# Optimization experiments

Measured on AMD Instinct MI355X. Metric: run time of the kernel, lower is better.

Reference implementation:

```python
import jax, jax.numpy as jnp
import numpy as np

B, N, E, T = 32768, 6, 6, 2  # batch graphs, nodes, edges (ring), edge types
H, DIN = 128, 3


def _ring_rel():
    # off_diag[i, (i+1)%N] = 1 -> edge e: sender i, receiver (i+1)%N
    send = np.arange(N)
    recv = (np.arange(N) + 1) % N
    eye = np.eye(N, dtype=np.float32)
    return jnp.asarray(eye[recv]), jnp.asarray(eye[send])  # rel_rec, rel_send [E,N]


def setup_inputs() -> dict:
    key = jax.random.key(0)
    ks = iter(jax.random.split(key, 40))
    rn = lambda shape, s=0.1: jax.random.normal(next(ks), shape, jnp.float32) * s
    rel_rec, rel_send = _ring_rel()
    inp = {
        'x': rn((B, N, DIN), 1.0),
        'rel_rec': rel_rec, 'rel_send': rel_send,
        'e1w1': rn((DIN, H)), 'e1b1': jnp.full((H,), 0.1), 'e1w2': rn((H, H)), 'e1b2': jnp.full((H,), 0.1),
        'e2w1': rn((2 * H, H)), 'e2b1': jnp.full((H,), 0.1), 'e2w2': rn((H, H)), 'e2b2': jnp.full((H,), 0.1),
        'e3w1': rn((H, H)), 'e3b1': jnp.full((H,), 0.1), 'e3w2': rn((H, H)), 'e3b2': jnp.full((H,), 0.1),
        'e4w1': rn((2 * H, H)), 'e4b1': jnp.full((H,), 0.1), 'e4w2': rn((H, H)), 'e4b2': jnp.full((H,), 0.1),
        'ew_out': rn((H, T)), 'eb_out': jnp.full((T,), 0.1),
        'd_msg_w1': rn((T, 2 * DIN, H)), 'd_msg_b1': rn((T, H), 0.01),
        'd_msg_w2': rn((T, H, H)), 'd_msg_b2': rn((T, H), 0.01),
        'd_out_w1': rn((DIN + H, H)), 'd_out_b1': rn((H,), 0.01),
        'd_out_w2': rn((H, H)), 'd_out_b2': rn((H,), 0.01),
        'd_out_w3': rn((H, DIN)), 'd_out_b3': rn((DIN,), 0.01),
    }
    return inp


def _mlp(h, w1, b1, w2, b2):
    # two-layer ELU MLP (dropout inactive at eval)
    return jax.nn.elu(jax.nn.elu(h @ w1 + b1) @ w2 + b2)


def reference(x, rel_rec, rel_send,
              e1w1, e1b1, e1w2, e1b2, e2w1, e2b1, e2w2, e2b2,
              e3w1, e3b1, e3w2, e3b2, e4w1, e4b1, e4w2, e4b2,
              ew_out, eb_out,
              d_msg_w1, d_msg_b1, d_msg_w2, d_msg_b2,
              d_out_w1, d_out_b1, d_out_w2, d_out_b2, d_out_w3, d_out_b3):
    node2edge = lambda h: jnp.concatenate(
        [jnp.einsum('en,bnh->beh', rel_rec, h), jnp.einsum('en,bnh->beh', rel_send, h)], axis=-1)

    # ---- GraphEncoder (factor=False) ----
    h = _mlp(x, e1w1, e1b1, e1w2, e1b2)                      # [B,N,H]
    he = _mlp(node2edge(h), e2w1, e2b1, e2w2, e2b2)          # [B,E,H]
    h2 = _mlp(he, e3w1, e3b1, e3w2, e3b2)                    # [B,E,H]
    h3 = _mlp(jnp.concatenate([h2, he], -1), e4w1, e4b1, e4w2, e4b2)
    logits = h3 @ ew_out + eb_out                            # [B,E,T]
    rel_type = jax.nn.softmax(logits, axis=-1)               # edge-type weights

    # ---- GraphDecoder single step (skip_first=False) ----
    recv = jnp.einsum('en,bnd->bed', rel_rec, x)             # [B,E,DIN]
    send = jnp.einsum('en,bnd->bed', rel_send, x)
    pre_msg = jnp.concatenate([recv, send], axis=-1)         # [B,E,2*DIN]
    # batched per-edge-type MLP: one grouped GEMM instead of a python loop of layers
    m = jax.nn.relu(jnp.einsum('bei,tih->bteh', pre_msg, d_msg_w1) + d_msg_b1[None, :, None, :])
    m = jax.nn.relu(jnp.einsum('bteh,tho->bteo', m, d_msg_w2) + d_msg_b2[None, :, None, :])
    all_msgs = jnp.einsum('bteh,bet->beh', m, rel_type)      # weight + accumulate over types
    agg_msgs = jnp.einsum('beh,en->bnh', all_msgs, rel_rec)  # edge -> node aggregation

    aug = jnp.concatenate([x, agg_msgs], axis=-1)            # [B,N,DIN+H]
    p = jax.nn.relu(aug @ d_out_w1 + d_out_b1)
    p = jax.nn.relu(p @ d_out_w2 + d_out_b2)
    p = p @ d_out_w3 + d_out_b3
    return x + p                                             # [B,N,DIN]
```

## Files before the change

### kernel.cpp

```cpp
#include <hip/hip_runtime.h>
#include <hip/hip_bf16.h>

typedef __bf16 bf16x8 __attribute__((ext_vector_type(8)));
typedef float floatx4 __attribute__((ext_vector_type(4)));

#define LDW 136
#define PXW 40

#define O_E1W2  0
#define O_E2W1  16384
#define O_E2W2  49152
#define O_E3W1  65536
#define O_E3W2  81920
#define O_E4W1  98304
#define O_E4W2  131072
#define O_DM2T0 147456
#define O_DM2T1 163840
#define O_DO1   180224
#define O_DO2   196608
#define O_EWOUT 212992
#define O_DW3   215040
#define O_E1W1P 217088
#define O_M1T0P 221184
#define O_M1T1P 225280
#define O_DO1XP 229376
#define WS_ELEMS 233472

__global__ void prep_kernel(const float* e1w2, const float* e2w1, const float* e2w2,
    const float* e3w1, const float* e3w2, const float* e4w1, const float* e4w2,
    const float* dmsg2, const float* dout1, const float* dout2,
    const float* ew_out, const float* dout_w3, const float* e1w1,
    const float* dmsg_w1, __hip_bfloat16* ws) {
  int idx = blockIdx.x * 256 + threadIdx.x;
  if (idx >= WS_ELEMS) return;
  float v;
  if (idx < O_E2W1)      { int l = idx;           v = e1w2[(l & 127) * 128 + (l >> 7)]; }
  else if (idx < O_E2W2) { int l = idx - O_E2W1;  v = e2w1[(l & 255) * 128 + (l >> 8)]; }
  else if (idx < O_E3W1) { int l = idx - O_E2W2;  v = e2w2[(l & 127) * 128 + (l >> 7)]; }
  else if (idx < O_E3W2) { int l = idx - O_E3W1;  v = e3w1[(l & 127) * 128 + (l >> 7)]; }
  else if (idx < O_E4W1) { int l = idx - O_E3W2;  v = e3w2[(l & 127) * 128 + (l >> 7)]; }
  else if (idx < O_E4W2) { int l = idx - O_E4W1;  v = e4w1[(l & 255) * 128 + (l >> 8)]; }
  else if (idx < O_DM2T0){ int l = idx - O_E4W2;  v = e4w2[(l & 127) * 128 + (l >> 7)]; }
  else if (idx < O_DM2T1){ int l = idx - O_DM2T0; v = dmsg2[(l & 127) * 128 + (l >> 7)]; }
  else if (idx < O_DO1)  { int l = idx - O_DM2T1; v = dmsg2[16384 + (l & 127) * 128 + (l >> 7)]; }
  else if (idx < O_DO2)  { int l = idx - O_DO1;   v = dout1[384 + (l & 127) * 128 + (l >> 7)]; }
  else if (idx < O_EWOUT){ int l = idx - O_DO2;   v = dout2[(l & 127) * 128 + (l >> 7)]; }
  else if (idx < O_DW3)  { int l = idx - O_EWOUT; int n = l >> 7;
                           v = (n < 2) ? ew_out[(l & 127) * 2 + n] : 0.f; }
  else if (idx < O_E1W1P){ int l = idx - O_DW3;   int n = l >> 7;
                           v = (n < 3) ? dout_w3[(l & 127) * 3 + n] : 0.f; }
  else if (idx < O_M1T0P){ int l = idx - O_E1W1P; int n = l >> 5, c = l & 31;
                           v = (c >= 3 && c < 6) ? e1w1[(c - 3) * 128 + n] : 0.f; }
  else if (idx < O_M1T1P){ int l = idx - O_M1T0P; int n = l >> 5, c = l & 31;
                           v = (c < 6) ? dmsg_w1[c * 128 + n] : 0.f; }
  else if (idx < O_DO1XP){ int l = idx - O_M1T1P; int n = l >> 5, c = l & 31;
                           v = (c < 6) ? dmsg_w1[768 + c * 128 + n] : 0.f; }
  else                   { int l = idx - O_DO1XP; int n = l >> 5, c = l & 31;
                           v = (c >= 3 && c < 6) ? dout1[(c - 3) * 128 + n] : 0.f; }
  ws[idx] = __float2bfloat16(v);
}

__global__ __launch_bounds__(256, 2) void nri_fused(
    const float* __restrict__ x,
    const float* __restrict__ e1b1, const float* __restrict__ e1b2,
    const float* __restrict__ e2b1, const float* __restrict__ e2b2,
    const float* __restrict__ e3b1, const float* __restrict__ e3b2,
    const float* __restrict__ e4b1, const float* __restrict__ e4b2,
    const float* __restrict__ eb_out,
    const float* __restrict__ dmsg_b1, const float* __restrict__ dmsg_b2,
    const float* __restrict__ dout_b1, const float* __restrict__ dout_b2,
    const float* __restrict__ dout_b3,
    const __bf16* __restrict__ wt, float* __restrict__ out)
{
  const int tid  = threadIdx.x;
  const int wave = tid >> 6;
  const int lane = tid & 63;
  const int nl   = lane & 15;
  const int quad = lane >> 4;
  const int gx   = blockIdx.x * 288;

  __shared__ __align__(16) __hip_bfloat16 bufA[96 * LDW];
  __shared__ __align__(16) __hip_bfloat16 bufB[96 * LDW];
  __shared__ __align__(16) __hip_bfloat16 pxb[96 * PXW];
  __shared__ __align__(16) float biasL[16 * 128];
  __shared__ float rtw[192];
  __shared__ float xs[288];
  __shared__ float obuf[288];

  for (int i = tid; i < 288; i += 256) xs[i] = x[gx + i];
  for (int i = tid; i < 2048; i += 256) {
    int row = i >> 7, c = i & 127;
    float v;
    switch (row) {
      case 0: v = e1b1[c]; break;   case 1: v = e1b2[c]; break;
      case 2: v = e2b1[c]; break;   case 3: v = e2b2[c]; break;
      case 4: v = e3b1[c]; break;   case 5: v = e3b2[c]; break;
      case 6: v = e4b1[c]; break;   case 7: v = e4b2[c]; break;
      case 8: v = dmsg_b1[c]; break;  case 9: v = dmsg_b1[128 + c]; break;
      case 10: v = dmsg_b2[c]; break; case 11: v = dmsg_b2[128 + c]; break;
      case 12: v = dout_b1[c]; break; case 13: v = dout_b2[c]; break;
      case 14: v = (c < 2) ? eb_out[c] : 0.f; break;
      default: v = (c < 3) ? dout_b3[c] : 0.f; break;
    }
    biasL[i] = v;
  }
  for (int i = tid; i < 96 * 32; i += 256) {
    int row = i >> 5, c = i & 31;
    int e = row % 6;
    float v = 0.f;
    if (c < 3)      { int rr = row + ((e == 5) ? -5 : 1); v = x[gx + rr * 3 + c]; }
    else if (c < 6) v = x[gx + row * 3 + (c - 3)];
    pxb[row * PXW + c] = __float2bfloat16(v);
  }
  __syncthreads();

  auto initb = [&](floatx4 (&a)[6][2], int brow) {
#pragma unroll
    for (int nt = 0; nt < 2; ++nt) {
      float bv = biasL[brow * 128 + wave * 32 + nt * 16 + nl];
      floatx4 v = {bv, bv, bv, bv};
#pragma unroll
      for (int mt = 0; mt < 6; ++mt) a[mt][nt] = v;
    }
  };

  auto gemm128 = [&](floatx4 (&acc)[6][2], const __hip_bfloat16* in, const __bf16* w) {
    const __bf16* ab = (const __bf16*)(const void*)in;
    const __bf16* w0 = w + (wave * 32 + nl) * 128 + quad * 8;
    const __bf16* w1 = w0 + 16 * 128;
#pragma unroll
    for (int ks = 0; ks < 4; ++ks) {
      int kk = ks * 32 + quad * 8;
      bf16x8 b0 = *(const bf16x8*)(w0 + ks * 32);
      bf16x8 b1 = *(const bf16x8*)(w1 + ks * 32);
#pragma unroll
      for (int mt = 0; mt < 6; ++mt) {
        bf16x8 a = *(const bf16x8*)(ab + (mt * 16 + nl) * LDW + kk);
        acc[mt][0] = __builtin_amdgcn_mfma_f32_16x16x32_bf16(a, b0, acc[mt][0], 0, 0, 0);
        acc[mt][1] = __builtin_amdgcn_mfma_f32_16x16x32_bf16(a, b1, acc[mt][1], 0, 0, 0);
      }
    }
  };

  auto gemm256 = [&](floatx4 (&acc)[6][2], const __hip_bfloat16* in0, bool recv0,
                     const __hip_bfloat16* in1, const __bf16* w) {
    int rofs0[6], rofs1[6];
#pragma unroll
    for (int mt = 0; mt < 6; ++mt) {
      int r = mt * 16 + nl;
      rofs1[mt] = r * LDW;
      if (recv0) { int e = r % 6; r += (e == 5) ? -5 : 1; }
      rofs0[mt] = r * LDW;
    }
    const __bf16* ab0 = (const __bf16*)(const void*)in0;
    const __bf16* ab1 = (const __bf16*)(const void*)in1;
    const __bf16* w0 = w + (wave * 32 + nl) * 256 + quad * 8;
    const __bf16* w1 = w0 + 16 * 256;
#pragma unroll
    for (int ks = 0; ks < 8; ++ks) {
      int kk = (ks & 3) * 32 + quad * 8;
      const __bf16* ab = (ks < 4) ? ab0 : ab1;
      const int* rofs = (ks < 4) ? rofs0 : rofs1;
      bf16x8 b0 = *(const bf16x8*)(w0 + ks * 32);
      bf16x8 b1 = *(const bf16x8*)(w1 + ks * 32);
#pragma unroll
      for (int mt = 0; mt < 6; ++mt) {
        bf16x8 a = *(const bf16x8*)(ab + rofs[mt] + kk);
        acc[mt][0] = __builtin_amdgcn_mfma_f32_16x16x32_bf16(a, b0, acc[mt][0], 0, 0, 0);
        acc[mt][1] = __builtin_amdgcn_mfma_f32_16x16x32_bf16(a, b1, acc[mt][1], 0, 0, 0);
      }
    }
  };

  auto gemm32 = [&](floatx4 (&acc)[6][2], int wofs) {
    const __bf16* pb = (const __bf16*)(const void*)pxb;
    const __bf16* wp = wt + wofs + (wave * 32 + nl) * 32 + quad * 8;
    bf16x8 b0 = *(const bf16x8*)(wp);
    bf16x8 b1 = *(const bf16x8*)(wp + 512);
#pragma unroll
    for (int mt = 0; mt < 6; ++mt) {
      bf16x8 a = *(const bf16x8*)(pb + (mt * 16 + nl) * PXW + quad * 8);
      acc[mt][0] = __builtin_amdgcn_mfma_f32_16x16x32_bf16(a, b0, acc[mt][0], 0, 0, 0);
      acc[mt][1] = __builtin_amdgcn_mfma_f32_16x16x32_bf16(a, b1, acc[mt][1], 0, 0, 0);
    }
  };

  auto store_act = [&](floatx4 (&acc)[6][2], int act, __hip_bfloat16* ob) {
#pragma unroll
    for (int nt = 0; nt < 2; ++nt) {
      int col = wave * 32 + nt * 16 + nl;
#pragma unroll
      for (int mt = 0; mt < 6; ++mt)
#pragma unroll
        for (int r = 0; r < 4; ++r) {
          float z = acc[mt][nt][r];
          if (act == 1) z = (z > 0.f) ? z : (__expf(z) - 1.f);
          else z = fmaxf(z, 0.f);
          ob[(mt * 16 + quad * 4 + r) * LDW + col] = __float2bfloat16(z);
        }
    }
  };

  floatx4 acc[6][2];

  initb(acc, 0); gemm32(acc, O_E1W1P); store_act(acc, 1, bufA);
  __syncthreads();
  initb(acc, 1); gemm128(acc, bufA, wt + O_E1W2); store_act(acc, 1, bufB);
  __syncthreads();
  initb(acc, 2); gemm256(acc, bufB, true, bufB, wt + O_E2W1); store_act(acc, 1, bufA);
  __syncthreads();
  initb(acc, 3); gemm128(acc, bufA, wt + O_E2W2); store_act(acc, 1, bufB);
  __syncthreads();
  initb(acc, 4); gemm128(acc, bufB, wt + O_E3W1); store_act(acc, 1, bufA);
  __syncthreads();
  initb(acc, 5); gemm128(acc, bufA, wt + O_E3W2);
  __syncthreads();
  store_act(acc, 1, bufA);
  __syncthreads();
  initb(acc, 6); gemm256(acc, bufA, false, bufB, wt + O_E4W1);
  __syncthreads();
  store_act(acc, 1, bufA);
  __syncthreads();
  initb(acc, 7); gemm128(acc, bufA, wt + O_E4W2); store_act(acc, 1, bufB);
  __syncthreads();

  if (wave < 3) {
#pragma unroll
    for (int tt = 0; tt < 2; ++tt) {
      int tile = wave * 2 + tt;
      float bv = biasL[14 * 128 + nl];
      floatx4 lg = {bv, bv, bv, bv};
      const __bf16* ab = (const __bf16*)(const void*)bufB;
      const __bf16* wp = wt + O_EWOUT + nl * 128 + quad * 8;
#pragma unroll
      for (int ks = 0; ks < 4; ++ks) {
        bf16x8 a = *(const bf16x8*)(ab + (tile * 16 + nl) * LDW + ks * 32 + quad * 8);
        bf16x8 b = *(const bf16x8*)(wp + ks * 32);
        lg = __builtin_amdgcn_mfma_f32_16x16x32_bf16(a, b, lg, 0, 0, 0);
      }
      if (nl < 2) {
#pragma unroll
        for (int r = 0; r < 4; ++r)
          rtw[(tile * 16 + quad * 4 + r) * 2 + nl] = lg[r];
      }
    }
  }
  __syncthreads();

  if (tid < 96) {
    float l0 = rtw[tid * 2], l1 = rtw[tid * 2 + 1];
    float mx = fmaxf(l0, l1);
    float ea = __expf(l0 - mx), eb = __expf(l1 - mx);
    float inv = 1.f / (ea + eb);
    rtw[tid * 2] = ea * inv; rtw[tid * 2 + 1] = eb * inv;
  }
  {
    floatx4 acc1[6][2];
    initb(acc, 8);  gemm32(acc, O_M1T0P);  store_act(acc, 2, bufA);
    initb(acc1, 9); gemm32(acc1, O_M1T1P); store_act(acc1, 2, bufB);
    __syncthreads();

    initb(acc, 10);  gemm128(acc, bufA, wt + O_DM2T0);
    initb(acc1, 11); gemm128(acc1, bufB, wt + O_DM2T1);
#pragma unroll
    for (int mt = 0; mt < 6; ++mt)
#pragma unroll
      for (int r = 0; r < 4; ++r) {
        int row = mt * 16 + quad * 4 + r;
        float r0 = rtw[row * 2], r1 = rtw[row * 2 + 1];
#pragma unroll
        for (int nt = 0; nt < 2; ++nt)
          acc[mt][nt][r] = r0 * fmaxf(acc[mt][nt][r], 0.f)
                         + r1 * fmaxf(acc1[mt][nt][r], 0.f);
      }
  }
  __syncthreads();

#pragma unroll
  for (int nt = 0; nt < 2; ++nt) {
    int col = wave * 32 + nt * 16 + nl;
#pragma unroll
    for (int mt = 0; mt < 6; ++mt)
#pragma unroll
      for (int r = 0; r < 4; ++r) {
        int row = mt * 16 + quad * 4 + r;
        int e = row % 6;
        int orow = row + ((e == 5) ? -5 : 1);
        bufA[orow * LDW + col] = __float2bfloat16(acc[mt][nt][r]);
      }
  }
  __syncthreads();

  initb(acc, 12); gemm128(acc, bufA, wt + O_DO1); gemm32(acc, O_DO1XP);
  store_act(acc, 2, bufB);
  __syncthreads();
  initb(acc, 13); gemm128(acc, bufB, wt + O_DO2); store_act(acc, 2, bufA);
  __syncthreads();

  if (wave < 3) {
#pragma unroll
    for (int tt = 0; tt < 2; ++tt) {
      int tile = wave * 2 + tt;
      float bv = biasL[15 * 128 + nl];
      floatx4 d = {bv, bv, bv, bv};
      const __bf16* ab = (const __bf16*)(const void*)bufA;
      const __bf16* wp = wt + O_DW3 + nl * 128 + quad * 8;
#pragma unroll
      for (int ks = 0; ks < 4; ++ks) {
        bf16x8 a = *(const bf16x8*)(ab + (tile * 16 + nl) * LDW + ks * 32 + quad * 8);
        bf16x8 b = *(const bf16x8*)(wp + ks * 32);
        d = __builtin_amdgcn_mfma_f32_16x16x32_bf16(a, b, d, 0, 0, 0);
      }
      if (nl < 3) {
#pragma unroll
        for (int r = 0; r < 4; ++r) {
          int row = tile * 16 + quad * 4 + r;
          obuf[row * 3 + nl] = xs[row * 3 + nl] + d[r];
        }
      }
    }
  }
  __syncthreads();
  for (int i = tid; i < 288; i += 256) out[gx + i] = obuf[i];
}

extern "C" void kernel_launch(void* const* d_in, const int* in_sizes, int n_in,
                              void* d_out, int out_size, void* d_ws, size_t ws_size,
                              hipStream_t stream) {
  const float* x       = (const float*)d_in[0];
  const float* e1w1    = (const float*)d_in[3];
  const float* e1b1    = (const float*)d_in[4];
  const float* e1w2    = (const float*)d_in[5];
  const float* e1b2    = (const float*)d_in[6];
  const float* e2w1    = (const float*)d_in[7];
  const float* e2b1    = (const float*)d_in[8];
  const float* e2w2    = (const float*)d_in[9];
  const float* e2b2    = (const float*)d_in[10];
  const float* e3w1    = (const float*)d_in[11];
  const float* e3b1    = (const float*)d_in[12];
  const float* e3w2    = (const float*)d_in[13];
  const float* e3b2    = (const float*)d_in[14];
  const float* e4w1    = (const float*)d_in[15];
  const float* e4b1    = (const float*)d_in[16];
  const float* e4w2    = (const float*)d_in[17];
  const float* e4b2    = (const float*)d_in[18];
  const float* ew_out  = (const float*)d_in[19];
  const float* eb_out  = (const float*)d_in[20];
  const float* dmsg_w1 = (const float*)d_in[21];
  const float* dmsg_b1 = (const float*)d_in[22];
  const float* dmsg_w2 = (const float*)d_in[23];
  const float* dmsg_b2 = (const float*)d_in[24];
  const float* dout_w1 = (const float*)d_in[25];
  const float* dout_b1 = (const float*)d_in[26];
  const float* dout_w2 = (const float*)d_in[27];
  const float* dout_b2 = (const float*)d_in[28];
  const float* dout_w3 = (const float*)d_in[29];
  const float* dout_b3 = (const float*)d_in[30];

  prep_kernel<<<(WS_ELEMS + 255) / 256, 256, 0, stream>>>(
      e1w2, e2w1, e2w2, e3w1, e3w2, e4w1, e4w2, dmsg_w2, dout_w1, dout_w2,
      ew_out, dout_w3, e1w1, dmsg_w1, (__hip_bfloat16*)d_ws);

  nri_fused<<<32768 / 16, 256, 0, stream>>>(
      x, e1b1, e1b2, e2b1, e2b2, e3b1, e3b2, e4b1, e4b2, eb_out,
      dmsg_b1, dmsg_b2, dout_b1, dout_b2, dout_b3,
      (const __bf16*)d_ws, (float*)d_out);
}
```

Baseline: 292.4 us.

## Split GEMM output columns across eight waves with 512-thread blocks

Doubles the block size from 256 to 512 threads so each of eight waves computes one 16-column tile instead of two, halving per-wave accumulators. The small logits and output projections now give one row tile to each of six waves rather than two tiles to each of three. The aim is more waves in flight per CU and lower register pressure, to better hide LDS and MFMA latency. In exchange, each A-fragment LDS read now feeds one MFMA instead of two, roughly doubling LDS read traffic per FLOP, and the 4-blocks-per-SM bound requests occupancy that the LDS footprint may not allow.

Measured after the change: 276.7 us. -5.4%, faster.

```diff
diff --git a/kernel.cpp b/kernel.cpp
--- a/kernel.cpp
+++ b/kernel.cpp
@@ -60,7 +60,7 @@
   ws[idx] = __float2bfloat16(v);
 }
 
-__global__ __launch_bounds__(256, 2) void nri_fused(
+__global__ __launch_bounds__(512, 4) void nri_fused(
     const float* __restrict__ x,
     const float* __restrict__ e1b1, const float* __restrict__ e1b2,
     const float* __restrict__ e2b1, const float* __restrict__ e2b2,
@@ -77,6 +77,7 @@
   const int lane = tid & 63;
   const int nl   = lane & 15;
   const int quad = lane >> 4;
+  const int colb = wave * 16 + nl;
   const int gx   = blockIdx.x * 288;
 
   __shared__ __align__(16) __hip_bfloat16 bufA[96 * LDW];
@@ -87,8 +88,8 @@
   __shared__ float xs[288];
   __shared__ float obuf[288];
 
-  for (int i = tid; i < 288; i += 256) xs[i] = x[gx + i];
-  for (int i = tid; i < 2048; i += 256) {
+  for (int i = tid; i < 288; i += 512) xs[i] = x[gx + i];
+  for (int i = tid; i < 2048; i += 512) {
     int row = i >> 7, c = i & 127;
     float v;
     switch (row) {
@@ -104,7 +105,7 @@
     }
     biasL[i] = v;
   }
-  for (int i = tid; i < 96 * 32; i += 256) {
+  for (int i = tid; i < 96 * 32; i += 512) {
     int row = i >> 5, c = i & 31;
     int e = row % 6;
     float v = 0.f;
@@ -114,35 +115,29 @@
   }
   __syncthreads();
 
-  auto initb = [&](floatx4 (&a)[6][2], int brow) {
-#pragma unroll
-    for (int nt = 0; nt < 2; ++nt) {
-      float bv = biasL[brow * 128 + wave * 32 + nt * 16 + nl];
-      floatx4 v = {bv, bv, bv, bv};
-#pragma unroll
-      for (int mt = 0; mt < 6; ++mt) a[mt][nt] = v;
-    }
-  };
-
-  auto gemm128 = [&](floatx4 (&acc)[6][2], const __hip_bfloat16* in, const __bf16* w) {
+  auto initb = [&](floatx4 (&a)[6], int brow) {
+    float bv = biasL[brow * 128 + colb];
+    floatx4 v = {bv, bv, bv, bv};
+#pragma unroll
+    for (int mt = 0; mt < 6; ++mt) a[mt] = v;
+  };
+
+  auto gemm128 = [&](floatx4 (&acc)[6], const __hip_bfloat16* in, const __bf16* w) {
     const __bf16* ab = (const __bf16*)(const void*)in;
-    const __bf16* w0 = w + (wave * 32 + nl) * 128 + quad * 8;
-    const __bf16* w1 = w0 + 16 * 128;
+    const __bf16* w0 = w + colb * 128 + quad * 8;
 #pragma unroll
     for (int ks = 0; ks < 4; ++ks) {
       int kk = ks * 32 + quad * 8;
       bf16x8 b0 = *(const bf16x8*)(w0 + ks * 32);
-      bf16x8 b1 = *(const bf16x8*)(w1 + ks * 32);
 #pragma unroll
       for (int mt = 0; mt < 6; ++mt) {
         bf16x8 a = *(const bf16x8*)(ab + (mt * 16 + nl) * LDW + kk);
-        acc[mt][0] = __builtin_amdgcn_mfma_f32_16x16x32_bf16(a, b0, acc[mt][0], 0, 0, 0);
-        acc[mt][1] = __builtin_amdgcn_mfma_f32_16x16x32_bf16(a, b1, acc[mt][1], 0, 0, 0);
-      }
-    }
-  };
-
-  auto gemm256 = [&](floatx4 (&acc)[6][2], const __hip_bfloat16* in0, bool recv0,
+        acc[mt] = __builtin_amdgcn_mfma_f32_16x16x32_bf16(a, b0, acc[mt], 0, 0, 0);
+      }
+    }
+  };
+
+  auto gemm256 = [&](floatx4 (&acc)[6], const __hip_bfloat16* in0, bool recv0,
                      const __hip_bfloat16* in1, const __bf16* w) {
     int rofs0[6], rofs1[6];
 #pragma unroll
@@ -154,54 +149,44 @@
     }
     const __bf16* ab0 = (const __bf16*)(const void*)in0;
     const __bf16* ab1 = (const __bf16*)(const void*)in1;
-    const __bf16* w0 = w + (wave * 32 + nl) * 256 + quad * 8;
-    const __bf16* w1 = w0 + 16 * 256;
+    const __bf16* w0 = w + colb * 256 + quad * 8;
 #pragma unroll
     for (int ks = 0; ks < 8; ++ks) {
       int kk = (ks & 3) * 32 + quad * 8;
       const __bf16* ab = (ks < 4) ? ab0 : ab1;
       const int* rofs = (ks < 4) ? rofs0 : rofs1;
       bf16x8 b0 = *(const bf16x8*)(w0 + ks * 32);
-      bf16x8 b1 = *(const bf16x8*)(w1 + ks * 32);
 #pragma unroll
       for (int mt = 0; mt < 6; ++mt) {
         bf16x8 a = *(const bf16x8*)(ab + rofs[mt] + kk);
-        acc[mt][0] = __builtin_amdgcn_mfma_f32_16x16x32_bf16(a, b0, acc[mt][0], 0, 0, 0);
-        acc[mt][1] = __builtin_amdgcn_mfma_f32_16x16x32_bf16(a, b1, acc[mt][1], 0, 0, 0);
-      }
-    }
-  };
-
-  auto gemm32 = [&](floatx4 (&acc)[6][2], int wofs) {
+        acc[mt] = __builtin_amdgcn_mfma_f32_16x16x32_bf16(a, b0, acc[mt], 0, 0, 0);
+      }
+    }
+  };
+
+  auto gemm32 = [&](floatx4 (&acc)[6], int wofs) {
     const __bf16* pb = (const __bf16*)(const void*)pxb;
-    const __bf16* wp = wt + wofs + (wave * 32 + nl) * 32 + quad * 8;
-    bf16x8 b0 = *(const bf16x8*)(wp);
-    bf16x8 b1 = *(const bf16x8*)(wp + 512);
+    bf16x8 b0 = *(const bf16x8*)(wt + wofs + colb * 32 + quad * 8);
 #pragma unroll
     for (int mt = 0; mt < 6; ++mt) {
       bf16x8 a = *(const bf16x8*)(pb + (mt * 16 + nl) * PXW + quad * 8);
-      acc[mt][0] = __builtin_amdgcn_mfma_f32_16x16x32_bf16(a, b0, acc[mt][0], 0, 0, 0);
-      acc[mt][1] = __builtin_amdgcn_mfma_f32_16x16x32_bf16(a, b1, acc[mt][1], 0, 0, 0);
-    }
-  };
-
-  auto store_act = [&](floatx4 (&acc)[6][2], int act, __hip_bfloat16* ob) {
-#pragma unroll
-    for (int nt = 0; nt < 2; ++nt) {
-      int col = wave * 32 + nt * 16 + nl;
-#pragma unroll
-      for (int mt = 0; mt < 6; ++mt)
-#pragma unroll
-        for (int r = 0; r < 4; ++r) {
-          float z = acc[mt][nt][r];
-          if (act == 1) z = (z > 0.f) ? z : (__expf(z) - 1.f);
-          else z = fmaxf(z, 0.f);
-          ob[(mt * 16 + quad * 4 + r) * LDW + col] = __float2bfloat16(z);
-        }
-    }
-  };
-
-  floatx4 acc[6][2];
+      acc[mt] = __builtin_amdgcn_mfma_f32_16x16x32_bf16(a, b0, acc[mt], 0, 0, 0);
+    }
+  };
+
+  auto store_act = [&](floatx4 (&acc)[6], int act, __hip_bfloat16* ob) {
+#pragma unroll
+    for (int mt = 0; mt < 6; ++mt)
+#pragma unroll
+      for (int r = 0; r < 4; ++r) {
+        float z = acc[mt][r];
+        if (act == 1) z = (z > 0.f) ? z : (__expf(z) - 1.f);
+        else z = fmaxf(z, 0.f);
+        ob[(mt * 16 + quad * 4 + r) * LDW + colb] = __float2bfloat16(z);
+      }
+  };
+
+  floatx4 acc[6];
 
   initb(acc, 0); gemm32(acc, O_E1W1P); store_act(acc, 1, bufA);
   __syncthreads();
@@ -224,25 +209,22 @@
   initb(acc, 7); gemm128(acc, bufA, wt + O_E4W2); store_act(acc, 1, bufB);
   __syncthreads();
 
-  if (wave < 3) {
-#pragma unroll
-    for (int tt = 0; tt < 2; ++tt) {
-      int tile = wave * 2 + tt;
-      float bv = biasL[14 * 128 + nl];
-      floatx4 lg = {bv, bv, bv, bv};
-      const __bf16* ab = (const __bf16*)(const void*)bufB;
-      const __bf16* wp = wt + O_EWOUT + nl * 128 + quad * 8;
-#pragma unroll
-      for (int ks = 0; ks < 4; ++ks) {
-        bf16x8 a = *(const bf16x8*)(ab + (tile * 16 + nl) * LDW + ks * 32 + quad * 8);
-        bf16x8 b = *(const bf16x8*)(wp + ks * 32);
-        lg = __builtin_amdgcn_mfma_f32_16x16x32_bf16(a, b, lg, 0, 0, 0);
-      }
-      if (nl < 2) {
-#pragma unroll
-        for (int r = 0; r < 4; ++r)
-          rtw[(tile * 16 + quad * 4 + r) * 2 + nl] = lg[r];
-      }
+  if (wave < 6) {
+    int tile = wave;
+    float bv = biasL[14 * 128 + nl];
+    floatx4 lg = {bv, bv, bv, bv};
+    const __bf16* ab = (const __bf16*)(const void*)bufB;
+    const __bf16* wp = wt + O_EWOUT + nl * 128 + quad * 8;
+#pragma unroll
+    for (int ks = 0; ks < 4; ++ks) {
+      bf16x8 a = *(const bf16x8*)(ab + (tile * 16 + nl) * LDW + ks * 32 + quad * 8);
+      bf16x8 b = *(const bf16x8*)(wp + ks * 32);
+      lg = __builtin_amdgcn_mfma_f32_16x16x32_bf16(a, b, lg, 0, 0, 0);
+    }
+    if (nl < 2) {
+#pragma unroll
+      for (int r = 0; r < 4; ++r)
+        rtw[(tile * 16 + quad * 4 + r) * 2 + nl] = lg[r];
     }
   }
   __syncthreads();
@@ -255,7 +237,7 @@
     rtw[tid * 2] = ea * inv; rtw[tid * 2 + 1] = eb * inv;
   }
   {
-    floatx4 acc1[6][2];
+    floatx4 acc1[6];
     initb(acc, 8);  gemm32(acc, O_M1T0P);  store_act(acc, 2, bufA);
     initb(acc1, 9); gemm32(acc1, O_M1T1P); store_act(acc1, 2, bufB);
     __syncthreads();
@@ -268,27 +250,20 @@
       for (int r = 0; r < 4; ++r) {
         int row = mt * 16 + quad * 4 + r;
         float r0 = rtw[row * 2], r1 = rtw[row * 2 + 1];
-#pragma unroll
-        for (int nt = 0; nt < 2; ++nt)
-          acc[mt][nt][r] = r0 * fmaxf(acc[mt][nt][r], 0.f)
-                         + r1 * fmaxf(acc1[mt][nt][r], 0.f);
-      }
-  }
-  __syncthreads();
-
-#pragma unroll
-  for (int nt = 0; nt < 2; ++nt) {
-    int col = wave * 32 + nt * 16 + nl;
-#pragma unroll
-    for (int mt = 0; mt < 6; ++mt)
-#pragma unroll
-      for (int r = 0; r < 4; ++r) {
-        int row = mt * 16 + quad * 4 + r;
-        int e = row % 6;
-        int orow = row + ((e == 5) ? -5 : 1);
-        bufA[orow * LDW + col] = __float2bfloat16(acc[mt][nt][r]);
-      }
-  }
+        acc[mt][r] = r0 * fmaxf(acc[mt][r], 0.f) + r1 * fmaxf(acc1[mt][r], 0.f);
+      }
+  }
+  __syncthreads();
+
+#pragma unroll
+  for (int mt = 0; mt < 6; ++mt)
+#pragma unroll
+    for (int r = 0; r < 4; ++r) {
+      int row = mt * 16 + quad * 4 + r;
+      int e = row % 6;
+      int orow = row + ((e == 5) ? -5 : 1);
+      bufA[orow * LDW + colb] = __float2bfloat16(acc[mt][r]);
+    }
   __syncthreads();
 
   initb(acc, 12); gemm128(acc, bufA, wt + O_DO1); gemm32(acc, O_DO1XP);
@@ -297,31 +272,28 @@
   initb(acc, 13); gemm128(acc, bufB, wt + O_DO2); store_act(acc, 2, bufA);
   __syncthreads();
 
-  if (wave < 3) {
-#pragma unroll
-    for (int tt = 0; tt < 2; ++tt) {
-      int tile = wave * 2 + tt;
-      float bv = biasL[15 * 128 + nl];
-      floatx4 d = {bv, bv, bv, bv};
-      const __bf16* ab = (const __bf16*)(const void*)bufA;
-      const __bf16* wp = wt + O_DW3 + nl * 128 + quad * 8;
-#pragma unroll
-      for (int ks = 0; ks < 4; ++ks) {
-        bf16x8 a = *(const bf16x8*)(ab + (tile * 16 + nl) * LDW + ks * 32 + quad * 8);
-        bf16x8 b = *(const bf16x8*)(wp + ks * 32);
-        d = __builtin_amdgcn_mfma_f32_16x16x32_bf16(a, b, d, 0, 0, 0);
-      }
-      if (nl < 3) {
-#pragma unroll
-        for (int r = 0; r < 4; ++r) {
-          int row = tile * 16 + quad * 4 + r;
-          obuf[row * 3 + nl] = xs[row * 3 + nl] + d[r];
-        }
-      }
-    }
-  }
-  __syncthreads();
-  for (int i = tid; i < 288; i += 256) out[gx + i] = obuf[i];
+  if (wave < 6) {
+    int tile = wave;
+    float bv = biasL[15 * 128 + nl];
+    floatx4 d = {bv, bv, bv, bv};
+    const __bf16* ab = (const __bf16*)(const void*)bufA;
+    const __bf16* wp = wt + O_DW3 + nl * 128 + quad * 8;
+#pragma unroll
+    for (int ks = 0; ks < 4; ++ks) {
+      bf16x8 a = *(const bf16x8*)(ab + (tile * 16 + nl) * LDW + ks * 32 + quad * 8);
+      bf16x8 b = *(const bf16x8*)(wp + ks * 32);
+      d = __builtin_amdgcn_mfma_f32_16x16x32_bf16(a, b, d, 0, 0, 0);
+    }
+    if (nl < 3) {
+#pragma unroll
+      for (int r = 0; r < 4; ++r) {
+        int row = tile * 16 + quad * 4 + r;
+        obuf[row * 3 + nl] = xs[row * 3 + nl] + d[r];
+      }
+    }
+  }
+  __syncthreads();
+  for (int i = tid; i < 288; i += 512) out[gx + i] = obuf[i];
 }
 
 extern "C" void kernel_launch(void* const* d_in, const int* in_sizes, int n_in,
@@ -361,7 +333,7 @@
       e1w2, e2w1, e2w2, e3w1, e3w2, e4w1, e4w2, dmsg_w2, dout_w1, dout_w2,
       ew_out, dout_w3, e1w1, dmsg_w1, (__hip_bfloat16*)d_ws);
 
-  nri_fused<<<32768 / 16, 256, 0, stream>>>(
+  nri_fused<<<32768 / 16, 512, 0, stream>>>(
       x, e1b1, e1b2, e2b1, e2b2, e3b1, e3b2, e4b1, e4b2, eb_out,
       dmsg_b1, dmsg_b2, dout_b1, dout_b2, dout_b3,
       (const __bf16*)d_ws, (float*)d_out);
```

## Split each block's GEMM tiles across eight waves instead of four

Applied to the files above, without the earlier changes.

The block grows from 256 to 512 threads. Each wave now computes a 48-row by 32-column tile (3x2 MFMA tiles) instead of 96x32, and waves are indexed by row-half and column-quarter. The logits and output-projection stages give one 16-row tile to each of six waves. The intent is more waves per block, fewer accumulator registers per wave and better latency hiding. In exchange, each wave reloads the same B-weight fragments for fewer rows, so weight traffic from global/L2 doubles, and the launch bounds now ask for 4 blocks of 512 threads per CU.

After: 346.2 us. 1.18x slower.

```diff
diff --git a/kernel.cpp b/kernel.cpp
--- a/kernel.cpp
+++ b/kernel.cpp
@@ -60,7 +60,7 @@
   ws[idx] = __float2bfloat16(v);
 }
 
-__global__ __launch_bounds__(256, 2) void nri_fused(
+__global__ __launch_bounds__(512, 4) void nri_fused(
     const float* __restrict__ x,
     const float* __restrict__ e1b1, const float* __restrict__ e1b2,
     const float* __restrict__ e2b1, const float* __restrict__ e2b2,
@@ -77,6 +77,8 @@
   const int lane = tid & 63;
   const int nl   = lane & 15;
   const int quad = lane >> 4;
+  const int rb   = (wave >> 2) * 48;
+  const int cb   = (wave & 3) * 32;
   const int gx   = blockIdx.x * 288;
 
   __shared__ __align__(16) __hip_bfloat16 bufA[96 * LDW];
@@ -87,8 +89,8 @@
   __shared__ float xs[288];
   __shared__ float obuf[288];
 
-  for (int i = tid; i < 288; i += 256) xs[i] = x[gx + i];
-  for (int i = tid; i < 2048; i += 256) {
+  for (int i = tid; i < 288; i += 512) xs[i] = x[gx + i];
+  for (int i = tid; i < 2048; i += 512) {
     int row = i >> 7, c = i & 127;
     float v;
     switch (row) {
@@ -104,7 +106,7 @@
     }
     biasL[i] = v;
   }
-  for (int i = tid; i < 96 * 32; i += 256) {
+  for (int i = tid; i < 96 * 32; i += 512) {
     int row = i >> 5, c = i & 31;
     int e = row % 6;
     float v = 0.f;
@@ -114,19 +116,19 @@
   }
   __syncthreads();
 
-  auto initb = [&](floatx4 (&a)[6][2], int brow) {
+  auto initb = [&](floatx4 (&a)[3][2], int brow) {
 #pragma unroll
     for (int nt = 0; nt < 2; ++nt) {
-      float bv = biasL[brow * 128 + wave * 32 + nt * 16 + nl];
+      float bv = biasL[brow * 128 + cb + nt * 16 + nl];
       floatx4 v = {bv, bv, bv, bv};
 #pragma unroll
-      for (int mt = 0; mt < 6; ++mt) a[mt][nt] = v;
-    }
-  };
-
-  auto gemm128 = [&](floatx4 (&acc)[6][2], const __hip_bfloat16* in, const __bf16* w) {
+      for (int mt = 0; mt < 3; ++mt) a[mt][nt] = v;
+    }
+  };
+
+  auto gemm128 = [&](floatx4 (&acc)[3][2], const __hip_bfloat16* in, const __bf16* w) {
     const __bf16* ab = (const __bf16*)(const void*)in;
-    const __bf16* w0 = w + (wave * 32 + nl) * 128 + quad * 8;
+    const __bf16* w0 = w + (cb + nl) * 128 + quad * 8;
     const __bf16* w1 = w0 + 16 * 128;
 #pragma unroll
     for (int ks = 0; ks < 4; ++ks) {
@@ -134,27 +136,27 @@
       bf16x8 b0 = *(const bf16x8*)(w0 + ks * 32);
       bf16x8 b1 = *(const bf16x8*)(w1 + ks * 32);
 #pragma unroll
-      for (int mt = 0; mt < 6; ++mt) {
-        bf16x8 a = *(const bf16x8*)(ab + (mt * 16 + nl) * LDW + kk);
+      for (int mt = 0; mt < 3; ++mt) {
+        bf16x8 a = *(const bf16x8*)(ab + (rb + mt * 16 + nl) * LDW + kk);
         acc[mt][0] = __builtin_amdgcn_mfma_f32_16x16x32_bf16(a, b0, acc[mt][0], 0, 0, 0);
         acc[mt][1] = __builtin_amdgcn_mfma_f32_16x16x32_bf16(a, b1, acc[mt][1], 0, 0, 0);
       }
     }
   };
 
-  auto gemm256 = [&](floatx4 (&acc)[6][2], const __hip_bfloat16* in0, bool recv0,
+  auto gemm256 = [&](floatx4 (&acc)[3][2], const __hip_bfloat16* in0, bool recv0,
                      const __hip_bfloat16* in1, const __bf16* w) {
-    int rofs0[6], rofs1[6];
-#pragma unroll
-    for (int mt = 0; mt < 6; ++mt) {
-      int r = mt * 16 + nl;
+    int rofs0[3], rofs1[3];
+#pragma unroll
+    for (int mt = 0; mt < 3; ++mt) {
+      int r = rb + mt * 16 + nl;
       rofs1[mt] = r * LDW;
       if (recv0) { int e = r % 6; r += (e == 5) ? -5 : 1; }
       rofs0[mt] = r * LDW;
     }
     const __bf16* ab0 = (const __bf16*)(const void*)in0;
     const __bf16* ab1 = (const __bf16*)(const void*)in1;
-    const __bf16* w0 = w + (wave * 32 + nl) * 256 + quad * 8;
+    const __bf16* w0 = w + (cb + nl) * 256 + quad * 8;
     const __bf16* w1 = w0 + 16 * 256;
 #pragma unroll
     for (int ks = 0; ks < 8; ++ks) {
@@ -164,7 +166,7 @@
       bf16x8 b0 = *(const bf16x8*)(w0 + ks * 32);
       bf16x8 b1 = *(const bf16x8*)(w1 + ks * 32);
 #pragma unroll
-      for (int mt = 0; mt < 6; ++mt) {
+      for (int mt = 0; mt < 3; ++mt) {
         bf16x8 a = *(const bf16x8*)(ab + rofs[mt] + kk);
         acc[mt][0] = __builtin_amdgcn_mfma_f32_16x16x32_bf16(a, b0, acc[mt][0], 0, 0, 0);
         acc[mt][1] = __builtin_amdgcn_mfma_f32_16x16x32_bf16(a, b1, acc[mt][1], 0, 0, 0);
@@ -172,36 +174,36 @@
     }
   };
 
-  auto gemm32 = [&](floatx4 (&acc)[6][2], int wofs) {
+  auto gemm32 = [&](floatx4 (&acc)[3][2], int wofs) {
     const __bf16* pb = (const __bf16*)(const void*)pxb;
-    const __bf16* wp = wt + wofs + (wave * 32 + nl) * 32 + quad * 8;
+    const __bf16* wp = wt + wofs + (cb + nl) * 32 + quad * 8;
     bf16x8 b0 = *(const bf16x8*)(wp);
     bf16x8 b1 = *(const bf16x8*)(wp + 512);
 #pragma unroll
-    for (int mt = 0; mt < 6; ++mt) {
-      bf16x8 a = *(const bf16x8*)(pb + (mt * 16 + nl) * PXW + quad * 8);
+    for (int mt = 0; mt < 3; ++mt) {
+      bf16x8 a = *(const bf16x8*)(pb + (rb + mt * 16 + nl) * PXW + quad * 8);
       acc[mt][0] = __builtin_amdgcn_mfma_f32_16x16x32_bf16(a, b0, acc[mt][0], 0, 0, 0);
       acc[mt][1] = __builtin_amdgcn_mfma_f32_16x16x32_bf16(a, b1, acc[mt][1], 0, 0, 0);
     }
   };
 
-  auto store_act = [&](floatx4 (&acc)[6][2], int act, __hip_bfloat16* ob) {
+  auto store_act = [&](floatx4 (&acc)[3][2], int act, __hip_bfloat16* ob) {
 #pragma unroll
     for (int nt = 0; nt < 2; ++nt) {
-      int col = wave * 32 + nt * 16 + nl;
-#pragma unroll
-      for (int mt = 0; mt < 6; ++mt)
+      int col = cb + nt * 16 + nl;
+#pragma unroll
+      for (int mt = 0; mt < 3; ++mt)
 #pragma unroll
         for (int r = 0; r < 4; ++r) {
           float z = acc[mt][nt][r];
           if (act == 1) z = (z > 0.f) ? z : (__expf(z) - 1.f);
           else z = fmaxf(z, 0.f);
-          ob[(mt * 16 + quad * 4 + r) * LDW + col] = __float2bfloat16(z);
+          ob[(rb + mt * 16 + quad * 4 + r) * LDW + col] = __float2bfloat16(z);
         }
     }
   };
 
-  floatx4 acc[6][2];
+  floatx4 acc[3][2];
 
   initb(acc, 0); gemm32(acc, O_E1W1P); store_act(acc, 1, bufA);
   __syncthreads();
@@ -224,25 +226,22 @@
   initb(acc, 7); gemm128(acc, bufA, wt + O_E4W2); store_act(acc, 1, bufB);
   __syncthreads();
 
-  if (wave < 3) {
-#pragma unroll
-    for (int tt = 0; tt < 2; ++tt) {
-      int tile = wave * 2 + tt;
-      float bv = biasL[14 * 128 + nl];
-      floatx4 lg = {bv, bv, bv, bv};
-      const __bf16* ab = (const __bf16*)(const void*)bufB;
-      const __bf16* wp = wt + O_EWOUT + nl * 128 + quad * 8;
-#pragma unroll
-      for (int ks = 0; ks < 4; ++ks) {
-        bf16x8 a = *(const bf16x8*)(ab + (tile * 16 + nl) * LDW + ks * 32 + quad * 8);
-        bf16x8 b = *(const bf16x8*)(wp + ks * 32);
-        lg = __builtin_amdgcn_mfma_f32_16x16x32_bf16(a, b, lg, 0, 0, 0);
-      }
-      if (nl < 2) {
-#pragma unroll
-        for (int r = 0; r < 4; ++r)
-          rtw[(tile * 16 + quad * 4 + r) * 2 + nl] = lg[r];
-      }
+  if (wave < 6) {
+    int tile = wave;
+    float bv = biasL[14 * 128 + nl];
+    floatx4 lg = {bv, bv, bv, bv};
+    const __bf16* ab = (const __bf16*)(const void*)bufB;
+    const __bf16* wp = wt + O_EWOUT + nl * 128 + quad * 8;
+#pragma unroll
+    for (int ks = 0; ks < 4; ++ks) {
+      bf16x8 a = *(const bf16x8*)(ab + (tile * 16 + nl) * LDW + ks * 32 + quad * 8);
+      bf16x8 b = *(const bf16x8*)(wp + ks * 32);
+      lg = __builtin_amdgcn_mfma_f32_16x16x32_bf16(a, b, lg, 0, 0, 0);
+    }
+    if (nl < 2) {
+#pragma unroll
+      for (int r = 0; r < 4; ++r)
+        rtw[(tile * 16 + quad * 4 + r) * 2 + nl] = lg[r];
     }
   }
   __syncthreads();
@@ -255,7 +254,7 @@
     rtw[tid * 2] = ea * inv; rtw[tid * 2 + 1] = eb * inv;
   }
   {
-    floatx4 acc1[6][2];
+    floatx4 acc1[3][2];
     initb(acc, 8);  gemm32(acc, O_M1T0P);  store_act(acc, 2, bufA);
     initb(acc1, 9); gemm32(acc1, O_M1T1P); store_act(acc1, 2, bufB);
     __syncthreads();
@@ -263,10 +262,10 @@
     initb(acc, 10);  gemm128(acc, bufA, wt + O_DM2T0);
     initb(acc1, 11); gemm128(acc1, bufB, wt + O_DM2T1);
 #pragma unroll
-    for (int mt = 0; mt < 6; ++mt)
+    for (int mt = 0; mt < 3; ++mt)
 #pragma unroll
       for (int r = 0; r < 4; ++r) {
-        int row = mt * 16 + quad * 4 + r;
+        int row = rb + mt * 16 + quad * 4 + r;
         float r0 = rtw[row * 2], r1 = rtw[row * 2 + 1];
 #pragma unroll
         for (int nt = 0; nt < 2; ++nt)
@@ -278,12 +277,12 @@
 
 #pragma unroll
   for (int nt = 0; nt < 2; ++nt) {
-    int col = wave * 32 + nt * 16 + nl;
-#pragma unroll
-    for (int mt = 0; mt < 6; ++mt)
+    int col = cb + nt * 16 + nl;
+#pragma unroll
+    for (int mt = 0; mt < 3; ++mt)
 #pragma unroll
       for (int r = 0; r < 4; ++r) {
-        int row = mt * 16 + quad * 4 + r;
+        int row = rb + mt * 16 + quad * 4 + r;
         int e = row % 6;
         int orow = row + ((e == 5) ? -5 : 1);
         bufA[orow * LDW + col] = __float2bfloat16(acc[mt][nt][r]);
@@ -297,31 +296,28 @@
   initb(acc, 13); gemm128(acc, bufB, wt + O_DO2); store_act(acc, 2, bufA);
   __syncthreads();
 
-  if (wave < 3) {
-#pragma unroll
-    for (int tt = 0; tt < 2; ++tt) {
-      int tile = wave * 2 + tt;
-      float bv = biasL[15 * 128 + nl];
-      floatx4 d = {bv, bv, bv, bv};
-      const __bf16* ab = (const __bf16*)(const void*)bufA;
-      const __bf16* wp = wt + O_DW3 + nl * 128 + quad * 8;
-#pragma unroll
-      for (int ks = 0; ks < 4; ++ks) {
-        bf16x8 a = *(const bf16x8*)(ab + (tile * 16 + nl) * LDW + ks * 32 + quad * 8);
-        bf16x8 b = *(const bf16x8*)(wp + ks * 32);
-        d = __builtin_amdgcn_mfma_f32_16x16x32_bf16(a, b, d, 0, 0, 0);
-      }
-      if (nl < 3) {
-#pragma unroll
-        for (int r = 0; r < 4; ++r) {
-          int row = tile * 16 + quad * 4 + r;
-          obuf[row * 3 + nl] = xs[row * 3 + nl] + d[r];
-        }
-      }
-    }
-  }
-  __syncthreads();
-  for (int i = tid; i < 288; i += 256) out[gx + i] = obuf[i];
+  if (wave < 6) {
+    int tile = wave;
+    float bv = biasL[15 * 128 + nl];
+    floatx4 d = {bv, bv, bv, bv};
+    const __bf16* ab = (const __bf16*)(const void*)bufA;
+    const __bf16* wp = wt + O_DW3 + nl * 128 + quad * 8;
+#pragma unroll
+    for (int ks = 0; ks < 4; ++ks) {
+      bf16x8 a = *(const bf16x8*)(ab + (tile * 16 + nl) * LDW + ks * 32 + quad * 8);
+      bf16x8 b = *(const bf16x8*)(wp + ks * 32);
+      d = __builtin_amdgcn_mfma_f32_16x16x32_bf16(a, b, d, 0, 0, 0);
+    }
+    if (nl < 3) {
+#pragma unroll
+      for (int r = 0; r < 4; ++r) {
+        int row = tile * 16 + quad * 4 + r;
+        obuf[row * 3 + nl] = xs[row * 3 + nl] + d[r];
+      }
+    }
+  }
+  __syncthreads();
+  for (int i = tid; i < 288; i += 512) out[gx + i] = obuf[i];
 }
 
 extern "C" void kernel_launch(void* const* d_in, const int* in_sizes, int n_in,
@@ -361,7 +357,7 @@
       e1w2, e2w1, e2w2, e3w1, e3w2, e4w1, e4w2, dmsg_w2, dout_w1, dout_w2,
       ew_out, dout_w3, e1w1, dmsg_w1, (__hip_bfloat16*)d_ws);
 
-  nri_fused<<<32768 / 16, 256, 0, stream>>>(
+  nri_fused<<<32768 / 16, 512, 0, stream>>>(
       x, e1b1, e1b2, e2b1, e2b2, e3b1, e3b2, e4b1, e4b2, eb_out,
       dmsg_b1, dmsg_b2, dout_b1, dout_b2, dout_b3,
       (const __bf16*)d_ws, (float*)d_out);
```
